# Optimization experiments

Hardware: AMD Instinct MI355X
Metric: run time of the kernel (lower is better)

## Reference

```python
import jax, jax.numpy as jnp
import numpy as np

DIM = 128
CODEBOOK_SIZE = 1024


def setup_inputs() -> dict:
    key = jax.random.key(0)
    kx, ke = jax.random.split(key)
    x = jax.random.normal(kx, (64, 1500, DIM), dtype=jnp.float32)
    # uniform_init uses kaiming_uniform_ on [K, D]: U(-b, b), b = sqrt(6 / fan_in) with a=sqrt(5) -> gain adjusts bound
    bound = float(np.sqrt(1.0 / DIM))  # kaiming_uniform with a=sqrt(5): bound = sqrt(6/((1+5)*fan_in)) = sqrt(1/fan_in)
    embed = jax.random.uniform(ke, (CODEBOOK_SIZE, DIM), dtype=jnp.float32, minval=-bound, maxval=bound)
    return {"x": x, "embed": embed}


def reference(x, embed):
    # x: [B, T, D], embed: [K, D]
    B, T, D = x.shape
    flat = x.reshape(-1, D)  # [N, D]
    dist = (2.0 * (flat @ embed.T)
            - jnp.sum(flat * flat, axis=-1, keepdims=True)
            - jnp.sum(embed * embed, axis=-1))  # [N, K]
    embed_ind = jnp.argmax(dist, axis=-1).reshape(B, T)  # [B, T]
    quantize = embed[embed_ind]  # [B, T, D] gather
    return quantize, embed_ind
```

## Files before the change

kernel.cpp:

```cpp
#include <hip/hip_runtime.h>
#include <hip/hip_fp16.h>

#define DIM 128
#define KCODES 1024
#define BROWS 128
#define NCH (KCODES / 16)
#define TAU_ACC 1.2e-3f

typedef _Float16 f16x8 __attribute__((ext_vector_type(8)));
typedef float f32x4 __attribute__((ext_vector_type(4)));

__global__ void enorm_kernel(const float* __restrict__ embed, float* __restrict__ enorm,
                             int* __restrict__ fcnt_g) {
    int k = blockIdx.x * blockDim.x + threadIdx.x;
    if (k == 0) *fcnt_g = 0;
    if (k < KCODES) {
        const float4* row = (const float4*)(embed + (size_t)k * DIM);
        float s = 0.f;
#pragma unroll
        for (int d = 0; d < DIM / 4; ++d) {
            float4 v = row[d];
            s = fmaf(v.x, v.x, s); s = fmaf(v.y, v.y, s);
            s = fmaf(v.z, v.z, s); s = fmaf(v.w, v.w, s);
        }
        enorm[k] = s;
    }
}

__global__ void pack_kernel(const float* __restrict__ embed, _Float16* __restrict__ Ehp) {
    int t = blockIdx.x * blockDim.x + threadIdx.x;
    int n  = t & 15;
    int q  = (t >> 4) & 3;
    int ks = (t >> 6) & 3;
    int c  = t >> 8;
    const float* src = embed + (size_t)(c * 16 + n) * DIM + ks * 32 + q * 8;
    float4 a0 = *(const float4*)src;
    float4 a1 = *(const float4*)(src + 4);
    float f[8] = {a0.x, a0.y, a0.z, a0.w, a1.x, a1.y, a1.z, a1.w};
    f16x8 h8;
#pragma unroll
    for (int j = 0; j < 8; ++j) h8[j] = (_Float16)f[j];
    *(f16x8*)&Ehp[(size_t)t * 8] = h8;
}

__global__ __launch_bounds__(256, 3)
void argmax_mfma_kernel(const float* __restrict__ x,
                        const _Float16* __restrict__ Ehp, const float* __restrict__ enorm,
                        float* __restrict__ outi, int* __restrict__ fcnt_g,
                        int* __restrict__ flags) {
    __shared__ float enorm_l[KCODES];

    const int tid  = threadIdx.x;
    const int w    = tid >> 6;
    const int lane = tid & 63;
    const int n    = lane & 15;
    const int q    = lane >> 4;
    const size_t row0 = (size_t)blockIdx.x * BROWS;

    {
        float4 e4 = ((const float4*)enorm)[tid];
        float4 v; v.x = -0.5f * e4.x; v.y = -0.5f * e4.y; v.z = -0.5f * e4.z; v.w = -0.5f * e4.w;
        ((float4*)enorm_l)[tid] = v;
    }

    const _Float16* EhpL = Ehp + (size_t)lane * 8;
    f16x8 bA0, bA1, bA2, bA3, bB0, bB1, bB2, bB3;
#define LOADB(P, B0, B1, B2, B3) do {                  \
    const _Float16* p_ = (P);                          \
    B0 = *(const f16x8*)(p_);                          \
    B1 = *(const f16x8*)(p_ + 512);                    \
    B2 = *(const f16x8*)(p_ + 1024);                   \
    B3 = *(const f16x8*)(p_ + 1536); } while (0)

    LOADB(EhpL, bA0, bA1, bA2, bA3);
    LOADB(EhpL + 2048, bB0, bB1, bB2, bB3);

    f16x8 xh[2][4], xl[2][4];
#pragma unroll
    for (int s = 0; s < 2; ++s)
#pragma unroll
        for (int ks = 0; ks < 4; ++ks) {
            const float* xp = x + (row0 + (size_t)(w * 32 + s * 16 + n)) * DIM + ks * 32 + q * 8;
            float4 a0 = *(const float4*)xp;
            float4 a1 = *(const float4*)(xp + 4);
            float f[8] = {a0.x, a0.y, a0.z, a0.w, a1.x, a1.y, a1.z, a1.w};
            f16x8 h, l;
#pragma unroll
            for (int j = 0; j < 8; ++j) {
                _Float16 hh = (_Float16)f[j];
                h[j] = hh;
                l[j] = (_Float16)(f[j] - (float)hh);
            }
            xh[s][ks] = h; xl[s][ks] = l;
        }

    __syncthreads();

    float best[2][4], sec[2][4]; int bidx[2][4];
#pragma unroll
    for (int s = 0; s < 2; ++s)
#pragma unroll
        for (int rg = 0; rg < 4; ++rg) { best[s][rg] = -3.4e38f; sec[s][rg] = -3.4e38f; bidx[s][rg] = 0; }

#define PROC(CI, B0, B1, B2, B3, EV) do {                                             \
    const int code_ = (CI) * 16 + n;                                                  \
    f32x4 h0 = {EV, EV, EV, EV}, l0 = {0.f, 0.f, 0.f, 0.f};                           \
    f32x4 h1 = {EV, EV, EV, EV}, l1 = {0.f, 0.f, 0.f, 0.f};                           \
    h0 = __builtin_amdgcn_mfma_f32_16x16x32_f16(xh[0][0], B0, h0, 0, 0, 0);           \
    h1 = __builtin_amdgcn_mfma_f32_16x16x32_f16(xh[1][0], B0, h1, 0, 0, 0);           \
    l0 = __builtin_amdgcn_mfma_f32_16x16x32_f16(xl[0][0], B0, l0, 0, 0, 0);           \
    l1 = __builtin_amdgcn_mfma_f32_16x16x32_f16(xl[1][0], B0, l1, 0, 0, 0);           \
    h0 = __builtin_amdgcn_mfma_f32_16x16x32_f16(xh[0][1], B1, h0, 0, 0, 0);           \
    h1 = __builtin_amdgcn_mfma_f32_16x16x32_f16(xh[1][1], B1, h1, 0, 0, 0);           \
    l0 = __builtin_amdgcn_mfma_f32_16x16x32_f16(xl[0][1], B1, l0, 0, 0, 0);           \
    l1 = __builtin_amdgcn_mfma_f32_16x16x32_f16(xl[1][1], B1, l1, 0, 0, 0);           \
    h0 = __builtin_amdgcn_mfma_f32_16x16x32_f16(xh[0][2], B2, h0, 0, 0, 0);           \
    h1 = __builtin_amdgcn_mfma_f32_16x16x32_f16(xh[1][2], B2, h1, 0, 0, 0);           \
    l0 = __builtin_amdgcn_mfma_f32_16x16x32_f16(xl[0][2], B2, l0, 0, 0, 0);           \
    l1 = __builtin_amdgcn_mfma_f32_16x16x32_f16(xl[1][2], B2, l1, 0, 0, 0);           \
    h0 = __builtin_amdgcn_mfma_f32_16x16x32_f16(xh[0][3], B3, h0, 0, 0, 0);           \
    h1 = __builtin_amdgcn_mfma_f32_16x16x32_f16(xh[1][3], B3, h1, 0, 0, 0);           \
    l0 = __builtin_amdgcn_mfma_f32_16x16x32_f16(xl[0][3], B3, l0, 0, 0, 0);           \
    l1 = __builtin_amdgcn_mfma_f32_16x16x32_f16(xl[1][3], B3, l1, 0, 0, 0);           \
    _Pragma("unroll")                                                                 \
    for (int rg = 0; rg < 4; ++rg) {                                                  \
        float sc0 = h0[rg] + l0[rg];                                                  \
        sec[0][rg]  = __builtin_amdgcn_fmed3f(best[0][rg], sec[0][rg], sc0);          \
        bidx[0][rg] = (sc0 > best[0][rg]) ? code_ : bidx[0][rg];                      \
        best[0][rg] = fmaxf(best[0][rg], sc0);                                        \
        float sc1 = h1[rg] + l1[rg];                                                  \
        sec[1][rg]  = __builtin_amdgcn_fmed3f(best[1][rg], sec[1][rg], sc1);          \
        bidx[1][rg] = (sc1 > best[1][rg]) ? code_ : bidx[1][rg];                      \
        best[1][rg] = fmaxf(best[1][rg], sc1);                                        \
    }                                                                                 \
} while (0)

    float eA = enorm_l[0 * 16 + n];
    float eB = enorm_l[1 * 16 + n];
#pragma unroll 1
    for (int cc = 0; cc < NCH; cc += 2) {
        float eA2 = enorm_l[((cc + 2) & (NCH - 1)) * 16 + n];
        float eB2 = enorm_l[((cc + 3) & (NCH - 1)) * 16 + n];
        const _Float16* p2 = EhpL + (size_t)((cc + 2) & (NCH - 1)) * 2048;
        const _Float16* p3 = EhpL + (size_t)((cc + 3) & (NCH - 1)) * 2048;
        PROC(cc, bA0, bA1, bA2, bA3, eA);
        LOADB(p2, bA0, bA1, bA2, bA3);
        PROC(cc + 1, bB0, bB1, bB2, bB3, eB);
        LOADB(p3, bB0, bB1, bB2, bB3);
        eA = eA2; eB = eB2;
    }
#undef PROC
#undef LOADB

#pragma unroll
    for (int mask = 1; mask < 16; mask <<= 1) {
#pragma unroll
        for (int s = 0; s < 2; ++s)
#pragma unroll
            for (int rg = 0; rg < 4; ++rg) {
                float ob = __shfl_xor(best[s][rg], mask);
                float os = __shfl_xor(sec[s][rg], mask);
                int   oi = __shfl_xor(bidx[s][rg], mask);
                if (ob > best[s][rg] || (ob == best[s][rg] && oi < bidx[s][rg])) {
                    sec[s][rg] = fmaxf(best[s][rg], os);
                    best[s][rg] = ob; bidx[s][rg] = oi;
                } else {
                    sec[s][rg] = fmaxf(sec[s][rg], ob);
                }
            }
    }
    if (n == 0) {
#pragma unroll
        for (int s = 0; s < 2; ++s)
#pragma unroll
            for (int rg = 0; rg < 4; ++rg) {
                int R = (int)row0 + w * 32 + s * 16 + q * 4 + rg;
                outi[R] = (float)bidx[s][rg];
                if (best[s][rg] - sec[s][rg] < TAU_ACC) {
                    int p = atomicAdd(fcnt_g, 1);
                    flags[p] = R;
                }
            }
    }
}

__global__ __launch_bounds__(256, 4)
void refine_kernel(const float* __restrict__ x, const float* __restrict__ embed,
                   const float* __restrict__ enorm, const int* __restrict__ fcnt_g,
                   const int* __restrict__ flags, float* __restrict__ outi) {
    __shared__ float rbest[4];
    __shared__ int   rbidx[4];
    const int tid  = threadIdx.x;
    const int w    = tid >> 6;
    const int lane = tid & 63;
    const int nf = *fcnt_g;
    for (int f = blockIdx.x; f < nf; f += gridDim.x) {
        int R = flags[f];
        const float4* xg4 = (const float4*)(x + (size_t)R * DIM);
        float b = -3.4e38f; int bi = 0;
        int cbase = tid * 4;
        for (int c = cbase; c < cbase + 4; ++c) {
            const float4* eg4 = (const float4*)(embed + (size_t)c * DIM);
            float s = 0.f;
#pragma unroll 8
            for (int d = 0; d < DIM / 4; ++d) {
                float4 xv = xg4[d], ev = eg4[d];
                s = fmaf(xv.x, ev.x, s); s = fmaf(xv.y, ev.y, s);
                s = fmaf(xv.z, ev.z, s); s = fmaf(xv.w, ev.w, s);
            }
            float sc = fmaf(2.f, s, -enorm[c]);
            if (sc > b) { b = sc; bi = c; }
        }
#pragma unroll
        for (int mask = 1; mask < 64; mask <<= 1) {
            float ob = __shfl_xor(b, mask);
            int   oi = __shfl_xor(bi, mask);
            if (ob > b || (ob == b && oi < bi)) { b = ob; bi = oi; }
        }
        if (lane == 0) { rbest[w] = b; rbidx[w] = bi; }
        __syncthreads();
        if (tid == 0) {
            float B = rbest[0]; int BI = rbidx[0];
#pragma unroll
            for (int i = 1; i < 4; ++i)
                if (rbest[i] > B || (rbest[i] == B && rbidx[i] < BI)) { B = rbest[i]; BI = rbidx[i]; }
            outi[R] = (float)BI;
        }
        __syncthreads();
    }
}

__global__ __launch_bounds__(256, 8)
void gather_kernel(const float* __restrict__ embed, const float* __restrict__ outi,
                   float* __restrict__ outq) {
    int g = blockIdx.x * 256 + threadIdx.x;
    int r = g >> 5, d4 = g & 31;
    int id = (int)outi[r];
    ((float4*)outq)[g] = ((const float4*)embed)[(size_t)id * (DIM / 4) + d4];
}

extern "C" void kernel_launch(void* const* d_in, const int* in_sizes, int n_in,
                              void* d_out, int out_size, void* d_ws, size_t ws_size,
                              hipStream_t stream) {
    const float* x     = (const float*)d_in[0];
    const float* embed = (const float*)d_in[1];
    const int x_elems  = in_sizes[0];
    const int n_rows   = x_elems / DIM;

    float*    enorm = (float*)d_ws;
    int*      fcnt  = (int*)((char*)d_ws + 4096);
    int*      flags = (int*)((char*)d_ws + 8192);
    _Float16* Ehp   = (_Float16*)((char*)d_ws + 8192 + n_rows * 4);

    float* outq = (float*)d_out;
    float* outi = (float*)d_out + (size_t)x_elems;

    enorm_kernel<<<KCODES / 256, 256, 0, stream>>>(embed, enorm, fcnt);
    pack_kernel<<<KCODES * 16 / 256, 256, 0, stream>>>(embed, Ehp);
    argmax_mfma_kernel<<<n_rows / BROWS, 256, 0, stream>>>(x, Ehp, enorm, outi, fcnt, flags);
    refine_kernel<<<2048, 256, 0, stream>>>(x, embed, enorm, fcnt, flags, outi);
    gather_kernel<<<n_rows * (DIM / 4) / 256, 256, 0, stream>>>(embed, outi, outq);
}
```

Before: 198.2 us.

## Merge prep kernels and fuse refine with gather via flagged-index encoding

Combines the codebook-norm and fp16 packing kernels into one launch. The argmax kernel now adds 0.5 to the stored index of ambiguous rows. A single epilogue kernel then gathers only unflagged rows, while extra blocks refine flagged rows and write both the corrected index and the gathered vector. This removes two kernel launches and the serialization between refine and gather. The cost is that refine and gather blocks share one grid, and the gather depends on the half-offset encoding in outi.

```diff
diff --git a/kernel.cpp b/kernel.cpp
--- a/kernel.cpp
+++ b/kernel.cpp
@@ -6,41 +6,45 @@
 #define BROWS 128
 #define NCH (KCODES / 16)
 #define TAU_ACC 1.2e-3f
+#define REF_BLOCKS 2048
 
 typedef _Float16 f16x8 __attribute__((ext_vector_type(8)));
 typedef float f32x4 __attribute__((ext_vector_type(4)));
 
-__global__ void enorm_kernel(const float* __restrict__ embed, float* __restrict__ enorm,
-                             int* __restrict__ fcnt_g) {
-    int k = blockIdx.x * blockDim.x + threadIdx.x;
-    if (k == 0) *fcnt_g = 0;
-    if (k < KCODES) {
-        const float4* row = (const float4*)(embed + (size_t)k * DIM);
-        float s = 0.f;
-#pragma unroll
-        for (int d = 0; d < DIM / 4; ++d) {
-            float4 v = row[d];
-            s = fmaf(v.x, v.x, s); s = fmaf(v.y, v.y, s);
-            s = fmaf(v.z, v.z, s); s = fmaf(v.w, v.w, s);
-        }
-        enorm[k] = s;
-    }
-}
-
-__global__ void pack_kernel(const float* __restrict__ embed, _Float16* __restrict__ Ehp) {
-    int t = blockIdx.x * blockDim.x + threadIdx.x;
-    int n  = t & 15;
-    int q  = (t >> 4) & 3;
-    int ks = (t >> 6) & 3;
-    int c  = t >> 8;
-    const float* src = embed + (size_t)(c * 16 + n) * DIM + ks * 32 + q * 8;
-    float4 a0 = *(const float4*)src;
-    float4 a1 = *(const float4*)(src + 4);
-    float f[8] = {a0.x, a0.y, a0.z, a0.w, a1.x, a1.y, a1.z, a1.w};
-    f16x8 h8;
-#pragma unroll
-    for (int j = 0; j < 8; ++j) h8[j] = (_Float16)f[j];
-    *(f16x8*)&Ehp[(size_t)t * 8] = h8;
+__global__ __launch_bounds__(256, 4)
+void prep_kernel(const float* __restrict__ embed, _Float16* __restrict__ Ehp,
+                 float* __restrict__ enorm, int* __restrict__ fcnt_g) {
+    const int bid = blockIdx.x;
+    const int tid = threadIdx.x;
+    if (bid < 64) {
+        int t = bid * 256 + tid;
+        int n  = t & 15;
+        int q  = (t >> 4) & 3;
+        int ks = (t >> 6) & 3;
+        int c  = t >> 8;
+        const float* src = embed + (size_t)(c * 16 + n) * DIM + ks * 32 + q * 8;
+        float4 a0 = *(const float4*)src;
+        float4 a1 = *(const float4*)(src + 4);
+        float f[8] = {a0.x, a0.y, a0.z, a0.w, a1.x, a1.y, a1.z, a1.w};
+        f16x8 h8;
+#pragma unroll
+        for (int j = 0; j < 8; ++j) h8[j] = (_Float16)f[j];
+        *(f16x8*)&Ehp[(size_t)t * 8] = h8;
+    } else {
+        int k = (bid - 64) * 256 + tid;
+        if (k == 0) *fcnt_g = 0;
+        if (k < KCODES) {
+            const float4* row = (const float4*)(embed + (size_t)k * DIM);
+            float s = 0.f;
+#pragma unroll
+            for (int d = 0; d < DIM / 4; ++d) {
+                float4 v = row[d];
+                s = fmaf(v.x, v.x, s); s = fmaf(v.y, v.y, s);
+                s = fmaf(v.z, v.z, s); s = fmaf(v.w, v.w, s);
+            }
+            enorm[k] = s;
+        }
+    }
 }
 
 __global__ __launch_bounds__(256, 3)
@@ -175,8 +179,9 @@
 #pragma unroll
             for (int rg = 0; rg < 4; ++rg) {
                 int R = (int)row0 + w * 32 + s * 16 + q * 4 + rg;
-                outi[R] = (float)bidx[s][rg];
-                if (best[s][rg] - sec[s][rg] < TAU_ACC) {
+                bool fl = (best[s][rg] - sec[s][rg] < TAU_ACC);
+                outi[R] = (float)bidx[s][rg] + (fl ? 0.5f : 0.0f);
+                if (fl) {
                     int p = atomicAdd(fcnt_g, 1);
                     flags[p] = R;
                 }
@@ -185,58 +190,68 @@
 }
 
 __global__ __launch_bounds__(256, 4)
-void refine_kernel(const float* __restrict__ x, const float* __restrict__ embed,
-                   const float* __restrict__ enorm, const int* __restrict__ fcnt_g,
-                   const int* __restrict__ flags, float* __restrict__ outi) {
-    __shared__ float rbest[4];
-    __shared__ int   rbidx[4];
-    const int tid  = threadIdx.x;
-    const int w    = tid >> 6;
-    const int lane = tid & 63;
-    const int nf = *fcnt_g;
-    for (int f = blockIdx.x; f < nf; f += gridDim.x) {
-        int R = flags[f];
-        const float4* xg4 = (const float4*)(x + (size_t)R * DIM);
-        float b = -3.4e38f; int bi = 0;
-        int cbase = tid * 4;
-        for (int c = cbase; c < cbase + 4; ++c) {
-            const float4* eg4 = (const float4*)(embed + (size_t)c * DIM);
-            float s = 0.f;
+void epilogue_kernel(const float* __restrict__ x, const float* __restrict__ embed,
+                     const float* __restrict__ enorm, const int* __restrict__ fcnt_g,
+                     const int* __restrict__ flags, float* __restrict__ outi,
+                     float* __restrict__ outq) {
+    const int bid = blockIdx.x;
+    const int tid = threadIdx.x;
+    const int gather_nb = gridDim.x - REF_BLOCKS;
+    if (bid < gather_nb) {
+        int g = bid * 256 + tid;
+        int r = g >> 5, d4 = g & 31;
+        float iv = outi[r];
+        if (iv == truncf(iv)) {
+            int id = (int)iv;
+            ((float4*)outq)[g] = ((const float4*)embed)[(size_t)id * (DIM / 4) + d4];
+        }
+    } else {
+        __shared__ float rbest[4];
+        __shared__ int   rbidx[4];
+        __shared__ int   sBI;
+        const int w    = tid >> 6;
+        const int lane = tid & 63;
+        const int nf = *fcnt_g;
+        for (int f = bid - gather_nb; f < nf; f += REF_BLOCKS) {
+            int R = flags[f];
+            const float4* xg4 = (const float4*)(x + (size_t)R * DIM);
+            float b = -3.4e38f; int bi = 0;
+            int cbase = tid * 4;
+            for (int c = cbase; c < cbase + 4; ++c) {
+                const float4* eg4 = (const float4*)(embed + (size_t)c * DIM);
+                float s = 0.f;
 #pragma unroll 8
-            for (int d = 0; d < DIM / 4; ++d) {
-                float4 xv = xg4[d], ev = eg4[d];
-                s = fmaf(xv.x, ev.x, s); s = fmaf(xv.y, ev.y, s);
-                s = fmaf(xv.z, ev.z, s); s = fmaf(xv.w, ev.w, s);
-            }
-            float sc = fmaf(2.f, s, -enorm[c]);
-            if (sc > b) { b = sc; bi = c; }
-        }
-#pragma unroll
-        for (int mask = 1; mask < 64; mask <<= 1) {
-            float ob = __shfl_xor(b, mask);
-            int   oi = __shfl_xor(bi, mask);
-            if (ob > b || (ob == b && oi < bi)) { b = ob; bi = oi; }
-        }
-        if (lane == 0) { rbest[w] = b; rbidx[w] = bi; }
-        __syncthreads();
-        if (tid == 0) {
-            float B = rbest[0]; int BI = rbidx[0];
-#pragma unroll
-            for (int i = 1; i < 4; ++i)
-                if (rbest[i] > B || (rbest[i] == B && rbidx[i] < BI)) { B = rbest[i]; BI = rbidx[i]; }
-            outi[R] = (float)BI;
-        }
-        __syncthreads();
-    }
-}
-
-__global__ __launch_bounds__(256, 8)
-void gather_kernel(const float* __restrict__ embed, const float* __restrict__ outi,
-                   float* __restrict__ outq) {
-    int g = blockIdx.x * 256 + threadIdx.x;
-    int r = g >> 5, d4 = g & 31;
-    int id = (int)outi[r];
-    ((float4*)outq)[g] = ((const float4*)embed)[(size_t)id * (DIM / 4) + d4];
+                for (int d = 0; d < DIM / 4; ++d) {
+                    float4 xv = xg4[d], ev = eg4[d];
+                    s = fmaf(xv.x, ev.x, s); s = fmaf(xv.y, ev.y, s);
+                    s = fmaf(xv.z, ev.z, s); s = fmaf(xv.w, ev.w, s);
+                }
+                float sc = fmaf(2.f, s, -enorm[c]);
+                if (sc > b) { b = sc; bi = c; }
+            }
+#pragma unroll
+            for (int mask = 1; mask < 64; mask <<= 1) {
+                float ob = __shfl_xor(b, mask);
+                int   oi = __shfl_xor(bi, mask);
+                if (ob > b || (ob == b && oi < bi)) { b = ob; bi = oi; }
+            }
+            if (lane == 0) { rbest[w] = b; rbidx[w] = bi; }
+            __syncthreads();
+            if (tid == 0) {
+                float B = rbest[0]; int BI = rbidx[0];
+#pragma unroll
+                for (int i = 1; i < 4; ++i)
+                    if (rbest[i] > B || (rbest[i] == B && rbidx[i] < BI)) { B = rbest[i]; BI = rbidx[i]; }
+                outi[R] = (float)BI;
+                sBI = BI;
+            }
+            __syncthreads();
+            if (tid < DIM / 4)
+                ((float4*)outq)[(size_t)R * (DIM / 4) + tid] =
+                    ((const float4*)embed)[(size_t)sBI * (DIM / 4) + tid];
+            __syncthreads();
+        }
+    }
 }
 
 extern "C" void kernel_launch(void* const* d_in, const int* in_sizes, int n_in,
@@ -255,9 +270,7 @@
     float* outq = (float*)d_out;
     float* outi = (float*)d_out + (size_t)x_elems;
 
-    enorm_kernel<<<KCODES / 256, 256, 0, stream>>>(embed, enorm, fcnt);
-    pack_kernel<<<KCODES * 16 / 256, 256, 0, stream>>>(embed, Ehp);
+    prep_kernel<<<64 + KCODES / 256, 256, 0, stream>>>(embed, Ehp, enorm, fcnt);
     argmax_mfma_kernel<<<n_rows / BROWS, 256, 0, stream>>>(x, Ehp, enorm, outi, fcnt, flags);
-    refine_kernel<<<2048, 256, 0, stream>>>(x, embed, enorm, fcnt, flags, outi);
-    gather_kernel<<<n_rows * (DIM / 4) / 256, 256, 0, stream>>>(embed, outi, outq);
-}
+    epilogue_kernel<<<n_rows / 8 + REF_BLOCKS, 256, 0, stream>>>(x, embed, enorm, fcnt, flags, outi, outq);
+}
```

After: 249.7 us. +26.0%, slower.
